# Kernel optimization log

Measured on AMD Instinct MI355X. Metric: run time of the kernel, lower is better.

## Reference

```python
import jax, jax.numpy as jnp
import numpy as np

N_GAS_NETS = 76  # 29 h2o + 13 o3 + 9 co2 + 3 n2o + 9 ch4 + 13 uniform
N_CHANNELS = 29
N_IN = 2   # (temperature, pressure)
H = 64     # hidden width per n_hidden=[64,64]

# gas index (into composition[0..5]) for each of the 76 stacked nets
COMP_IDX = jnp.asarray(np.repeat(np.arange(6), [29, 13, 9, 3, 9, 13]))

# sparse per-channel combine (hard-coded in the original forward)
H2O_IDX = jnp.asarray([0,1,2,3,4,5,6,3,4,9,10,11,12,13,14,15,16,17,18,19,20,21,22,23,24,25,26,27,28])
O3_CH  = jnp.asarray([0,1,2,17,18,19,20,21,22,25,26,27,28])
CO2_CH = jnp.asarray([0,1,2,5,6,9,10,13,14])
N2O_CH = jnp.asarray([0,1,2])
CH4_CH = jnp.asarray([0,1,2,3,4,7,8,11,12])
U_CH   = jnp.asarray([0,1,2,15,16,17,18,19,20,21,22,27,28])


def setup_inputs() -> dict:
    key = jax.random.key(0)
    ks = jax.random.split(key, 10)
    N = 32768
    t_p = jax.random.normal(ks[0], (N, N_IN), dtype=jnp.float32)
    composition = jax.random.uniform(ks[1], (8, N, 1), dtype=jnp.float32)
    s1 = 1.0 / np.sqrt(N_IN)
    s2 = 1.0 / np.sqrt(H)
    W1 = jax.random.normal(ks[2], (N_GAS_NETS, N_IN, H), dtype=jnp.float32) * s1
    b1 = jnp.zeros((N_GAS_NETS, H), dtype=jnp.float32)
    W2 = jax.random.normal(ks[3], (N_GAS_NETS, H, H), dtype=jnp.float32) * s2
    b2 = jnp.zeros((N_GAS_NETS, H), dtype=jnp.float32)
    Wout = jax.random.normal(ks[4], (N_GAS_NETS, H, 1), dtype=jnp.float32) * s2
    bout = jnp.zeros((N_GAS_NETS, 1), dtype=jnp.float32)
    ke_lw = jax.random.uniform(ks[5], (N_CHANNELS, 1), dtype=jnp.float32)
    ke_iw = jax.random.uniform(ks[6], (N_CHANNELS, 1), dtype=jnp.float32)
    return {"t_p": t_p, "composition": composition, "W1": W1, "b1": b1,
            "W2": W2, "b2": b2, "Wout": Wout, "bout": bout,
            "ke_lw": ke_lw, "ke_iw": ke_iw}


def reference(t_p, composition, W1, b1, W2, b2, Wout, bout, ke_lw, ke_iw):
    # Batched evaluation of all 76 tiny DenseFFN experts on the shared t_p input.
    h = jax.nn.relu(jnp.einsum('ni,gih->gnh', t_p, W1) + b1[:, None, :])   # [76,N,H]
    h = jax.nn.relu(jnp.einsum('gnh,ghk->gnk', h, W2) + b2[:, None, :])    # [76,N,H]
    ke = jax.nn.relu(jnp.einsum('gnh,gho->gno', h, Wout) + bout[:, None, :])  # [76,N,1]

    # tau_gas[gas] = ke * composition[gas_index]
    tau_all = ke * composition[COMP_IDX]  # [76,N,1]
    h2o = tau_all[0:29]
    o3 = tau_all[29:42]
    co2 = tau_all[42:51]
    n2o = tau_all[51:54]
    ch4 = tau_all[54:63]
    u = tau_all[63:76]

    # hard-coded sparse per-channel sum
    tau_gases = h2o[H2O_IDX]                      # [29,N,1]
    tau_gases = tau_gases.at[O3_CH].add(o3)
    tau_gases = tau_gases.at[CO2_CH].add(co2)
    tau_gases = tau_gases.at[N2O_CH].add(n2o)
    tau_gases = tau_gases.at[CH4_CH].add(ch4)
    tau_gases = tau_gases.at[U_CH].add(u)

    tau_lw = ke_lw[:, None, :] * composition[6]   # [29,N,1]
    tau_iw = ke_iw[:, None, :] * composition[7]   # [29,N,1]
    return (tau_gases, tau_lw, tau_iw)
```

## Files before the change

kernel.cpp:

```cpp
#include <hip/hip_runtime.h>

#define NPTS 32768

typedef _Float16 f16;
typedef _Float16 f16x2 __attribute__((ext_vector_type(2)));
typedef _Float16 f16x8 __attribute__((ext_vector_type(8)));
typedef float f32x2 __attribute__((ext_vector_type(2)));
typedef float f32x4 __attribute__((ext_vector_type(4)));

union H8 { f16x8 v8; f16x2 v2[4]; };

static __device__ __forceinline__ f16x2 pk_fma(f16x2 a, f16x2 b, f16x2 c) {
  return __builtin_elementwise_fma(a, b, c);
}
static __device__ __forceinline__ f16x2 pk_relu(f16x2 a) {
  f16x2 z = {(f16)0.f, (f16)0.f};
  return __builtin_elementwise_max(a, z);
}

__global__ __launch_bounds__(256, 2) void k1_mlp(
    const float* __restrict__ t_p, const float* __restrict__ W1,
    const float* __restrict__ b1, const float* __restrict__ W2,
    const float* __restrict__ b2, const float* __restrict__ Wout,
    const float* __restrict__ bout, float* __restrict__ kews)
{
  const int lane = threadIdx.x & 63;
  const int l15  = lane & 15;
  const int quad = lane >> 4;
  const int w    = blockIdx.x * 4 + (threadIdx.x >> 6);
  const int gi   = w >> 6;
  const int g    = gi + (gi >= 7 ? 2 : 0);
  const int pb0  = (w & 63) * 512;

  H8 afrag[4][2];
  const float* W2g = W2 + g * 4096;
  #pragma unroll
  for (int mt = 0; mt < 4; ++mt) {
    #pragma unroll
    for (int ks = 0; ks < 2; ++ks) {
      const float* src = W2g + (ks * 32 + quad * 8) * 64 + mt * 16 + l15;
      #pragma unroll
      for (int i = 0; i < 4; ++i) {
        f16x2 t = { (f16)src[(2 * i) * 64], (f16)src[(2 * i + 1) * 64] };
        afrag[mt][ks].v2[i] = t;
      }
    }
  }

  f16x2 w0h[2][4], w1h[2][4], b1h[2][4];
  const float* W1g = W1 + g * 128;
  const float* b1g = b1 + g * 64;
  #pragma unroll
  for (int ks = 0; ks < 2; ++ks) {
    #pragma unroll
    for (int i = 0; i < 4; ++i) {
      int h = ks * 32 + quad * 8 + 2 * i;
      w0h[ks][i] = f16x2{ (f16)W1g[h],      (f16)W1g[h + 1] };
      w1h[ks][i] = f16x2{ (f16)W1g[64 + h], (f16)W1g[64 + h + 1] };
      b1h[ks][i] = f16x2{ (f16)b1g[h],      (f16)b1g[h + 1] };
    }
  }

  f32x4 b2q[4];
  f32x2 wq2[4][2];
  #pragma unroll
  for (int mt = 0; mt < 4; ++mt) {
    b2q[mt] = *(const f32x4*)(b2 + g * 64 + mt * 16 + quad * 4);
    f32x4 wv = *(const f32x4*)(Wout + g * 64 + mt * 16 + quad * 4);
    wq2[mt][0] = f32x2{ wv[0], wv[1] };
    wq2[mt][1] = f32x2{ wv[2], wv[3] };
  }
  const float bo = bout[g];

  const float2* tp2 = (const float2*)t_p;
  float* outg = kews + g * NPTS;

  for (int pass = 0; pass < 8; ++pass) {
    const int pb = pb0 + pass * 64;

    float2 xv[4];
    #pragma unroll
    for (int pt = 0; pt < 4; ++pt)
      xv[pt] = tp2[pb + pt * 16 + l15];

    f16x2 x0v[4], x1v[4];
    #pragma unroll
    for (int pt = 0; pt < 4; ++pt) {
      f16 x0 = (f16)xv[pt].x, x1 = (f16)xv[pt].y;
      x0v[pt] = f16x2{ x0, x0 };
      x1v[pt] = f16x2{ x1, x1 };
    }

    H8 bfrag[2][4];
    #pragma unroll
    for (int ks = 0; ks < 2; ++ks)
      #pragma unroll
      for (int pt = 0; pt < 4; ++pt)
        #pragma unroll
        for (int i = 0; i < 4; ++i)
          bfrag[ks][pt].v2[i] =
              pk_relu(pk_fma(x0v[pt], w0h[ks][i], pk_fma(x1v[pt], w1h[ks][i], b1h[ks][i])));

    f32x4 acc[4][4];
    #pragma unroll
    for (int mt = 0; mt < 4; ++mt)
      #pragma unroll
      for (int pt = 0; pt < 4; ++pt) {
        f32x4 c0 = __builtin_amdgcn_mfma_f32_16x16x32_f16(
            afrag[mt][0].v8, bfrag[0][pt].v8, b2q[mt], 0, 0, 0);
        acc[mt][pt] = __builtin_amdgcn_mfma_f32_16x16x32_f16(
            afrag[mt][1].v8, bfrag[1][pt].v8, c0, 0, 0, 0);
      }

    float ke[4];
    #pragma unroll
    for (int pt = 0; pt < 4; ++pt) {
      f32x2 p2 = { 0.f, 0.f };
      #pragma unroll
      for (int mt = 0; mt < 4; ++mt) {
        f32x2 z = { 0.f, 0.f };
        f32x2 a0 = { acc[mt][pt][0], acc[mt][pt][1] };
        f32x2 a1 = { acc[mt][pt][2], acc[mt][pt][3] };
        a0 = __builtin_elementwise_max(a0, z);
        a1 = __builtin_elementwise_max(a1, z);
        p2 = __builtin_elementwise_fma(a0, wq2[mt][0], p2);
        p2 = __builtin_elementwise_fma(a1, wq2[mt][1], p2);
      }
      float p = p2[0] + p2[1];
      p += __shfl_xor(p, 16, 64);
      p += __shfl_xor(p, 32, 64);
      ke[pt] = fmaxf(p + bo, 0.f);
    }
    float v = (quad == 0) ? ke[0] : (quad == 1) ? ke[1] : (quad == 2) ? ke[2] : ke[3];
    outg[pb + lane] = v;
  }
}

__device__ const int CCNT[29] = { 6,6,6,2,2,2,2,2,2,2,2,2,2,2,2,2,2,3,3,3,3,3,3,1,1,2,2,3,3 };
__device__ const int CG[29][6] = {
  {0,29,42,51,54,63}, {1,30,43,52,55,64}, {2,31,44,53,56,65},
  {3,57,0,0,0,0},  {4,58,0,0,0,0},  {5,45,0,0,0,0},  {6,46,0,0,0,0},
  {3,59,0,0,0,0},  {4,60,0,0,0,0},  {9,47,0,0,0,0},  {10,48,0,0,0,0},
  {11,61,0,0,0,0}, {12,62,0,0,0,0}, {13,49,0,0,0,0}, {14,50,0,0,0,0},
  {15,66,0,0,0,0}, {16,67,0,0,0,0},
  {17,32,68,0,0,0}, {18,33,69,0,0,0}, {19,34,70,0,0,0},
  {20,35,71,0,0,0}, {21,36,72,0,0,0}, {22,37,73,0,0,0},
  {23,0,0,0,0,0},  {24,0,0,0,0,0},
  {25,38,0,0,0,0}, {26,39,0,0,0,0},
  {27,40,74,0,0,0}, {28,41,75,0,0,0}
};

__global__ __launch_bounds__(256) void k2_gather(
    const float* __restrict__ ws, const float* __restrict__ comp,
    const float* __restrict__ ke_lw, const float* __restrict__ ke_iw,
    float* __restrict__ out)
{
  const int c = blockIdx.x >> 7;
  const int n = ((blockIdx.x & 127) << 8) + threadIdx.x;

  float a = 0.f;
  const int cnt = CCNT[c];
  for (int i = 0; i < cnt; ++i) {
    int g = CG[c][i];
    int t = (g < 29) ? 0 : (g < 42) ? 1 : (g < 51) ? 2 : (g < 54) ? 3 : (g < 63) ? 4 : 5;
    a += ws[g * NPTS + n] * comp[t * NPTS + n];
  }
  out[c * NPTS + n] = a;
  out[29 * NPTS + c * NPTS + n] = ke_lw[c] * comp[6 * NPTS + n];
  out[58 * NPTS + c * NPTS + n] = ke_iw[c] * comp[7 * NPTS + n];
}

extern "C" void kernel_launch(void* const* d_in, const int* in_sizes, int n_in,
                              void* d_out, int out_size, void* d_ws, size_t ws_size,
                              hipStream_t stream)
{
  const float* t_p   = (const float*)d_in[0];
  const float* comp  = (const float*)d_in[1];
  const float* W1    = (const float*)d_in[2];
  const float* b1    = (const float*)d_in[3];
  const float* W2    = (const float*)d_in[4];
  const float* b2    = (const float*)d_in[5];
  const float* Wout  = (const float*)d_in[6];
  const float* bout  = (const float*)d_in[7];
  const float* ke_lw = (const float*)d_in[8];
  const float* ke_iw = (const float*)d_in[9];
  float* out = (float*)d_out;
  float* ws  = (float*)d_ws;

  k1_mlp<<<1184, 256, 0, stream>>>(t_p, W1, b1, W2, b2, Wout, bout, ws);
  k2_gather<<<29 * 128, 256, 0, stream>>>(ws, comp, ke_lw, ke_iw, out);
}
```

Measured before the change: 114.6 us.

## Fuse composition multiply and channel scatter into MLP kernel via atomics

Removes the intermediate per-net workspace and the gather kernel. The MLP kernel now multiplies each expert output by its composition row and atomically adds it into one or two output channels. A new init kernel zeroes the gas channels and writes the lw/iw outputs beforehand. This avoids writing and re-reading 74 workspace rows, but adds float atomics, which make summation order nondeterministic and may contend when several nets hit the same channel.

```diff
diff --git a/kernel.cpp b/kernel.cpp
--- a/kernel.cpp
+++ b/kernel.cpp
@@ -18,11 +18,49 @@
   return __builtin_elementwise_max(a, z);
 }
 
+__device__ const unsigned char G_T[74] = {
+  0,0,0,0,0,0,0, 0,0,0,0,0,0,0,0,0,0,0,0,0,0,0,0,0,0,0,0,
+  1,1,1,1,1,1,1,1,1,1,1,1,1,
+  2,2,2,2,2,2,2,2,2,
+  3,3,3,
+  4,4,4,4,4,4,4,4,4,
+  5,5,5,5,5,5,5,5,5,5,5,5,5
+};
+__device__ const unsigned char G_C1[74] = {
+  0,1,2,3,4,5,6, 9,10,11,12,13,14,15,16,17,18,19,20,21,22,23,24,25,26,27,28,
+  0,1,2,17,18,19,20,21,22,25,26,27,28,
+  0,1,2,5,6,9,10,13,14,
+  0,1,2,
+  0,1,2,3,4,7,8,11,12,
+  0,1,2,15,16,17,18,19,20,21,22,27,28
+};
+__device__ const unsigned char G_C2[74] = {
+  255,255,255,7,8,255,255, 255,255,255,255,255,255,255,255,255,255,255,255,
+  255,255,255,255,255,255,255,255,
+  255,255,255,255,255,255,255,255,255,255,255,255,255,
+  255,255,255,255,255,255,255,255,255,
+  255,255,255,
+  255,255,255,255,255,255,255,255,255,
+  255,255,255,255,255,255,255,255,255,255,255,255,255
+};
+
+__global__ __launch_bounds__(256) void k0_init(
+    const float* __restrict__ comp, const float* __restrict__ ke_lw,
+    const float* __restrict__ ke_iw, float* __restrict__ out)
+{
+  const int c = blockIdx.x >> 7;
+  const int n = ((blockIdx.x & 127) << 8) + threadIdx.x;
+  out[c * NPTS + n] = 0.f;
+  out[29 * NPTS + c * NPTS + n] = ke_lw[c] * comp[6 * NPTS + n];
+  out[58 * NPTS + c * NPTS + n] = ke_iw[c] * comp[7 * NPTS + n];
+}
+
 __global__ __launch_bounds__(256, 2) void k1_mlp(
-    const float* __restrict__ t_p, const float* __restrict__ W1,
-    const float* __restrict__ b1, const float* __restrict__ W2,
-    const float* __restrict__ b2, const float* __restrict__ Wout,
-    const float* __restrict__ bout, float* __restrict__ kews)
+    const float* __restrict__ t_p, const float* __restrict__ comp,
+    const float* __restrict__ W1, const float* __restrict__ b1,
+    const float* __restrict__ W2, const float* __restrict__ b2,
+    const float* __restrict__ Wout, const float* __restrict__ bout,
+    float* __restrict__ out)
 {
   const int lane = threadIdx.x & 63;
   const int l15  = lane & 15;
@@ -32,6 +70,10 @@
   const int g    = gi + (gi >= 7 ? 2 : 0);
   const int pb0  = (w & 63) * 512;
 
+  const int t  = G_T[gi];
+  const int c1 = G_C1[gi];
+  const int c2 = G_C2[gi];
+
   H8 afrag[4][2];
   const float* W2g = W2 + g * 4096;
   #pragma unroll
@@ -41,8 +83,8 @@
       const float* src = W2g + (ks * 32 + quad * 8) * 64 + mt * 16 + l15;
       #pragma unroll
       for (int i = 0; i < 4; ++i) {
-        f16x2 t = { (f16)src[(2 * i) * 64], (f16)src[(2 * i + 1) * 64] };
-        afrag[mt][ks].v2[i] = t;
+        f16x2 tt = { (f16)src[(2 * i) * 64], (f16)src[(2 * i + 1) * 64] };
+        afrag[mt][ks].v2[i] = tt;
       }
     }
   }
@@ -73,7 +115,9 @@
   const float bo = bout[g];
 
   const float2* tp2 = (const float2*)t_p;
-  float* outg = kews + g * NPTS;
+  const float* compt = comp + t * NPTS;
+  float* out1 = out + c1 * NPTS;
+  float* out2 = (c2 == 255) ? nullptr : out + c2 * NPTS;
 
   for (int pass = 0; pass < 8; ++pass) {
     const int pb = pb0 + pass * 64;
@@ -82,6 +126,7 @@
     #pragma unroll
     for (int pt = 0; pt < 4; ++pt)
       xv[pt] = tp2[pb + pt * 16 + l15];
+    const float cv = compt[pb + lane];
 
     f16x2 x0v[4], x1v[4];
     #pragma unroll
@@ -132,42 +177,10 @@
       ke[pt] = fmaxf(p + bo, 0.f);
     }
     float v = (quad == 0) ? ke[0] : (quad == 1) ? ke[1] : (quad == 2) ? ke[2] : ke[3];
-    outg[pb + lane] = v;
-  }
-}
-
-__device__ const int CCNT[29] = { 6,6,6,2,2,2,2,2,2,2,2,2,2,2,2,2,2,3,3,3,3,3,3,1,1,2,2,3,3 };
-__device__ const int CG[29][6] = {
-  {0,29,42,51,54,63}, {1,30,43,52,55,64}, {2,31,44,53,56,65},
-  {3,57,0,0,0,0},  {4,58,0,0,0,0},  {5,45,0,0,0,0},  {6,46,0,0,0,0},
-  {3,59,0,0,0,0},  {4,60,0,0,0,0},  {9,47,0,0,0,0},  {10,48,0,0,0,0},
-  {11,61,0,0,0,0}, {12,62,0,0,0,0}, {13,49,0,0,0,0}, {14,50,0,0,0,0},
-  {15,66,0,0,0,0}, {16,67,0,0,0,0},
-  {17,32,68,0,0,0}, {18,33,69,0,0,0}, {19,34,70,0,0,0},
-  {20,35,71,0,0,0}, {21,36,72,0,0,0}, {22,37,73,0,0,0},
-  {23,0,0,0,0,0},  {24,0,0,0,0,0},
-  {25,38,0,0,0,0}, {26,39,0,0,0,0},
-  {27,40,74,0,0,0}, {28,41,75,0,0,0}
-};
-
-__global__ __launch_bounds__(256) void k2_gather(
-    const float* __restrict__ ws, const float* __restrict__ comp,
-    const float* __restrict__ ke_lw, const float* __restrict__ ke_iw,
-    float* __restrict__ out)
-{
-  const int c = blockIdx.x >> 7;
-  const int n = ((blockIdx.x & 127) << 8) + threadIdx.x;
-
-  float a = 0.f;
-  const int cnt = CCNT[c];
-  for (int i = 0; i < cnt; ++i) {
-    int g = CG[c][i];
-    int t = (g < 29) ? 0 : (g < 42) ? 1 : (g < 51) ? 2 : (g < 54) ? 3 : (g < 63) ? 4 : 5;
-    a += ws[g * NPTS + n] * comp[t * NPTS + n];
-  }
-  out[c * NPTS + n] = a;
-  out[29 * NPTS + c * NPTS + n] = ke_lw[c] * comp[6 * NPTS + n];
-  out[58 * NPTS + c * NPTS + n] = ke_iw[c] * comp[7 * NPTS + n];
+    float tau = v * cv;
+    atomicAdd(&out1[pb + lane], tau);
+    if (out2) atomicAdd(&out2[pb + lane], tau);
+  }
 }
 
 extern "C" void kernel_launch(void* const* d_in, const int* in_sizes, int n_in,
@@ -185,8 +198,7 @@
   const float* ke_lw = (const float*)d_in[8];
   const float* ke_iw = (const float*)d_in[9];
   float* out = (float*)d_out;
-  float* ws  = (float*)d_ws;
-
-  k1_mlp<<<1184, 256, 0, stream>>>(t_p, W1, b1, W2, b2, Wout, bout, ws);
-  k2_gather<<<29 * 128, 256, 0, stream>>>(ws, comp, ke_lw, ke_iw, out);
-}
+
+  k0_init<<<29 * 128, 256, 0, stream>>>(comp, ke_lw, ke_iw, out);
+  k1_mlp<<<1184, 256, 0, stream>>>(t_p, comp, W1, b1, W2, b2, Wout, bout, out);
+}
```

Result: no change. 113.8 us (-0.7%).
